# Kernel optimization log

Hardware: AMD Instinct MI355X
Metric: run time of the kernel (lower is better)

The kernel has to match this reference:

```python
import jax, jax.numpy as jnp
import numpy as np

H = 256
LATENT = 128
NODE_FEATS = (12, 5, 4)
EDGE_FEATS = (5, 4)
END_NODE = NODE_FEATS[0] - 1
MAX_NODES = 64


def setup_inputs() -> dict:
    key = jax.random.key(0)
    ks = iter(jax.random.split(key, 40))
    def rn(shape, s=0.1):
        return jax.random.normal(next(ks), shape, dtype=jnp.float32) * s
    inp = {
        "z": jax.random.normal(next(ks), (1, LATENT), dtype=jnp.float32),
        "lp_w": rn((H, LATENT)), "lp_b": rn((H,)),
        "nWih": rn((3 * H, H)), "nWhh": rn((3 * H, H)), "nbih": rn((3 * H,)), "nbhh": rn((3 * H,)),
        "eWih": rn((3 * H, H)), "eWhh": rn((3 * H, H)), "ebih": rn((3 * H,)), "ebhh": rn((3 * H,)),
    }
    for j, f in enumerate(NODE_FEATS):
        inp[f"nc{j}_w"] = rn((f, H)); inp[f"nc{j}_b"] = rn((f,))
    for j, f in enumerate(EDGE_FEATS):
        inp[f"ec{j}_w"] = rn((f, H)); inp[f"ec{j}_b"] = rn((f,))
    inp["max_nodes"] = MAX_NODES
    return inp


def _gru(x, h, Wih, Whh, bih, bhh):
    # torch.nn.GRU single step, single layer. x,h: (1,H)
    gi = x @ Wih.T + bih
    gh = h @ Whh.T + bhh
    ir, iz, inn = jnp.split(gi, 3, axis=-1)
    hr, hz, hn = jnp.split(gh, 3, axis=-1)
    r = jax.nn.sigmoid(ir + hr)
    zg = jax.nn.sigmoid(iz + hz)
    n = jnp.tanh(inn + r * hn)
    return (1.0 - zg) * n + zg * h


def _classify(emb, W, b):
    # Linear -> softmax -> (max prob, argmax), batch=1 -> scalars
    p = jax.nn.softmax(emb @ W.T + b, axis=-1)[0]
    return jnp.max(p), jnp.argmax(p)


def _generate(z, lp_w, lp_b, nWih, nWhh, nbih, nbhh, eWih, eWhh, ebih, ebhh,
              nc0_w, nc0_b, nc1_w, nc1_b, nc2_w, nc2_b,
              ec0_w, ec0_b, ec1_w, ec1_b, max_nodes):
    node_cls = ((nc0_w, nc0_b), (nc1_w, nc1_b), (nc2_w, nc2_b))
    edge_cls = ((ec0_w, ec0_b), (ec1_w, ec1_b))
    h0 = z @ lp_w.T + lp_b                     # latent_project; set_context
    buf0 = jnp.zeros((max_nodes, 1, H), z.dtype)  # node embedding history

    def step(carry, i):
        h, buf, done = carry
        x = jnp.where(i == 0, jnp.zeros((1, H), z.dtype), buf[jnp.maximum(i - 1, 0)])
        h1 = _gru(x, h, nWih, nWhh, nbih, nbhh)   # node_celli.forward_unit; emb = h1
        nps, nis = zip(*[_classify(h1, W, b) for W, b in node_cls])
        nprobs = jnp.stack(nps)                   # (3,)
        nidxs = jnp.stack(nis)                    # (3,) int
        is_end = nidxs[0] == END_NODE

        # edge cell: seq over previous node embeddings, most recent first
        def estep(he, t):
            valid = t < i
            src = jnp.clip(i - 1 - t, 0, max_nodes - 1)
            he2 = _gru(buf[src], he, eWih, eWhh, ebih, ebhh)
            he_new = jnp.where(valid, he2, he)
            eps, eis = zip(*[_classify(he_new, W, b) for W, b in edge_cls])
            return he_new, (jnp.stack(eps), jnp.stack(eis))

        he_fin, (ep_t, ei_t) = jax.lax.scan(estep, h1, jnp.arange(max_nodes))
        # reindex: edge for source node j was produced at inner step t = i-1-j
        js = jnp.arange(max_nodes)
        ts = jnp.clip(i - 1 - js, 0, max_nodes - 1)
        ep_row = ep_t[ts]                          # (max_nodes, 2)
        ei_row = ei_t[ts]
        vj = js < i
        no_edges = jnp.all(jnp.where(vj, ei_row[:, 0] == 0, True)) & (i > 0)

        active = jnp.logical_not(done)
        node_ok = active & jnp.logical_not(is_end) & jnp.logical_not(no_edges)
        done_new = done | is_end | no_edges

        h_next = jnp.where(node_ok & (i > 0), he_fin, h1)  # node hidden <- edge hidden
        h_next = jnp.where(active, h_next, h)
        buf_new = buf.at[i].set(jnp.where(node_ok, h1, buf[i]))

        edge_valid = vj & node_ok & (i > 0)
        out = (jnp.where(node_ok, nprobs, 0.0), nidxs, node_ok,
               jnp.where(edge_valid[:, None], ep_row, 0.0), ei_row, edge_valid)
        return (h_next, buf_new, done_new), out

    _, outs = jax.lax.scan(step, (h0, buf0, jnp.zeros((), bool)), jnp.arange(max_nodes))
    # node_probs (M,3), node_idxs (M,3), node_valid (M,),
    # edge_probs (M,M,2), edge_idxs (M,M,2), edge_valid (M,M)
    return outs


def reference(z, lp_w, lp_b, nWih, nWhh, nbih, nbhh, eWih, eWhh, ebih, ebhh,
              nc0_w, nc0_b, nc1_w, nc1_b, nc2_w, nc2_b,
              ec0_w, ec0_b, ec1_w, ec1_b, max_nodes):
    return _generate(z, lp_w, lp_b, nWih, nWhh, nbih, nbhh, eWih, eWhh, ebih, ebhh,
                     nc0_w, nc0_b, nc1_w, nc1_b, nc2_w, nc2_b,
                     ec0_w, ec0_b, ec1_w, ec1_b, max_nodes)
```

## Files before the change

### kernel.cpp

```cpp
#include <hip/hip_runtime.h>
#include <stdint.h>
#include <cstddef>


typedef unsigned int u32;

#define H 256
#define HL 128
#define G3 768
#define NW 16
#define SL 16
#define MAXN 64
#define NSTATE (1 + MAXN + (MAXN*(MAXN-1))/2)
#define SENTU 0xFFFFFFFFu
#define DEADV 0x0000DEADu
#define PAD 264

#define WG_CLS NW
#define WG_HELP0 (NW+1)
#define NHELP_PER 6
#define NROLE (WG_HELP0 + 2*NHELP_PER)
#define NWG 256

#define NP_OFF 0
#define NI_OFF 192
#define NV_OFF 384
#define EP_OFF 448
#define EI_OFF (EP_OFF + MAXN*MAXN*2)
#define EV_OFF (EI_OFF + MAXN*MAXN*2)

struct Wksp {
  float hP[NSTATE][H];
  float hS[NSTATE][H];
  float gi_e[MAXN][G3];
  float gi_n[MAXN][G3];
  u32 decP[MAXN];
  u32 decS[MAXN];
  u32 winner;
  u32 padw[7];
  u32 ticket[8];
};

union Shm {
  struct {
    float whe[3*SL*PAD];
    float whn[3*SL*PAD];
    float hcur[2][H];
    float bihe[3*SL], bhhe[3*SL], bihn[3*SL], bhhn[3*SL];
    float zv[HL];
    u32 dec;
  } w;
  struct {
    float cw[30*H];
    float cb[30];
    float hc[2][H];
    float logits[32];
    float np[3]; int ni[3];
    float ept[MAXN][2];
    int   eit[MAXN][2];
    u32 isend, bflag;
  } c;
  struct { float h1[H]; } hp;
};

__device__ __forceinline__ u32 ld_sc0(const u32* p) {
  u32 v;
  asm volatile("global_load_dword %0, %1, off sc0\n\ts_waitcnt vmcnt(0)"
               : "=&v"(v) : "v"(p) : "memory");
  return v;
}
__device__ __forceinline__ void st_sc0(u32* p, u32 v) {
  asm volatile("global_store_dword %0, %1, off sc0" :: "v"(p), "v"(v) : "memory");
}
__device__ __forceinline__ u32 ld_ag(const u32* p) {
  return __hip_atomic_load(p, __ATOMIC_RELAXED, __HIP_MEMORY_SCOPE_AGENT);
}
__device__ __forceinline__ void st_ag(u32* p, u32 v) {
  __hip_atomic_store(p, v, __ATOMIC_RELAXED, __HIP_MEMORY_SCOPE_AGENT);
}
__device__ __forceinline__ void pub2(u32* pp, u32* sp, u32 v, bool sc) {
  if (sc) st_sc0(pp, v);
  st_ag(sp, v);
}
__device__ __forceinline__ u32 spin2(const u32* pp, const u32* sp, bool sc) {
  if (sc) {
    #pragma unroll 1
    for (int i = 0; i < 16; ++i) {
      const u32 v = ld_sc0(pp);
      if (v != SENTU) return v;
    }
  }
  u32 v = ld_ag(sp);
  while (v == SENTU) v = ld_ag(sp);
  return v;
}
__device__ __forceinline__ float spin2f(const float* pp, const float* sp, bool sc) {
  return __uint_as_float(spin2((const u32*)pp, (const u32*)sp, sc));
}
__device__ __forceinline__ float spinf(const float* p) {
  u32 v = ld_ag((const u32*)p);
  while (v == SENTU) v = ld_ag((const u32*)p);
  return __uint_as_float(v);
}
__device__ __forceinline__ float spinf_slow(const float* p) {
  u32 v = ld_ag((const u32*)p);
  while (v == SENTU) {
    __builtin_amdgcn_s_sleep(1);
    v = ld_ag((const u32*)p);
  }
  return __uint_as_float(v);
}
__device__ __forceinline__ void pubf(float* p, float x) { st_ag((u32*)p, __float_as_uint(x)); }
__device__ __forceinline__ float sigm(float x) { return 1.0f / (1.0f + expf(-x)); }

__global__ __launch_bounds__(256)
void Generator_34746285425383_kernel(
    const float* __restrict__ z, const float* __restrict__ lp_w, const float* __restrict__ lp_b,
    const float* __restrict__ nWih, const float* __restrict__ nWhh,
    const float* __restrict__ nbih, const float* __restrict__ nbhh,
    const float* __restrict__ eWih, const float* __restrict__ eWhh,
    const float* __restrict__ ebih, const float* __restrict__ ebhh,
    const float* __restrict__ nc0w, const float* __restrict__ nc0b,
    const float* __restrict__ nc1w, const float* __restrict__ nc1b,
    const float* __restrict__ nc2w, const float* __restrict__ nc2b,
    const float* __restrict__ ec0w, const float* __restrict__ ec0b,
    const float* __restrict__ ec1w, const float* __restrict__ ec1b,
    float* __restrict__ out, Wksp* __restrict__ ws)
{
  __shared__ Shm S;
  __shared__ int role_s, mode_s;
  const int tid = threadIdx.x;

  if (tid == 0) {
    u32 xcc;
    asm volatile("s_getreg_b32 %0, hwreg(HW_REG_XCC_ID)" : "=s"(xcc));
    xcc &= 7u;
    const u32 slot = __hip_atomic_fetch_add(&ws->ticket[xcc], 1u,
                        __ATOMIC_RELAXED, __HIP_MEMORY_SCOPE_AGENT);
    if (slot == NROLE - 1) {
      u32 exp = SENTU;
      __hip_atomic_compare_exchange_strong(&ws->winner, &exp, xcc,
          __ATOMIC_RELAXED, __ATOMIC_RELAXED, __HIP_MEMORY_SCOPE_AGENT);
    }
    u32 wv = ld_ag(&ws->winner);
    int iters = 0;
    while (wv == SENTU) {
      ++iters;
      if (iters > 1500 && blockIdx.x == 0) {
        u32 exp = SENTU;
        __hip_atomic_compare_exchange_strong(&ws->winner, &exp, DEADV,
            __ATOMIC_RELAXED, __ATOMIC_RELAXED, __HIP_MEMORY_SCOPE_AGENT);
      }
      wv = ld_ag(&ws->winner);
    }
    if (wv <= 7u) { role_s = (wv == xcc && slot < NROLE) ? (int)slot : -1; mode_s = 1; }
    else          { role_s = ((int)blockIdx.x < NROLE) ? (int)blockIdx.x : -1; mode_s = 0; }
  }
  __syncthreads();
  const int bid = role_s;
  const bool sc = (mode_s != 0);
  if (bid < 0) return;

  if (bid < NW) {
    const int w = bid, g = tid >> 4, c = tid & 15;
    const int k = w * SL + g;
    const bool gl = (c < 2);
    for (int r = 0; r < 3 * SL; ++r) {
      const int gate = r / SL, gg = r % SL;
      const int grow = gate * H + (w * SL + gg);
      for (int col = tid; col < H; col += 256) {
        S.w.whe[r * PAD + col] = eWhh[grow * H + col];
        S.w.whn[r * PAD + col] = nWhh[grow * H + col];
      }
    }
    if (tid < 3 * SL) {
      const int gate = tid / SL, gg = tid % SL;
      const int grow = gate * H + w * SL + gg;
      S.w.bihe[tid] = ebih[grow]; S.w.bhhe[tid] = ebhh[grow];
      S.w.bihn[tid] = nbih[grow]; S.w.bhhn[tid] = nbhh[grow];
    }
    if (tid < HL) S.w.zv[tid] = z[tid];
    __syncthreads();

    {
      float p = 0.f;
      for (int it = 0; it < 8; ++it) {
        const int col = c + 16 * it;
        p += S.w.zv[col] * lp_w[k * HL + col];
      }
      for (int off = 1; off < 16; off <<= 1) p += __shfl_xor(p, off);
      const float h0 = p + lp_b[k];
      if (c == 0 && sc) st_sc0((u32*)&ws->hP[0][k], __float_as_uint(h0));
      if (c == 1)       st_ag((u32*)&ws->hS[0][k], __float_as_uint(h0));
    }

    int m = 1, idx_carry = 0;
    bool done = false;
    unsigned long long valid = 0ull;
    float pg0 = 0.f, pg1 = 0.f, pg2 = 0.f;
    const float* pga = nullptr;

    for (int i = 0; i < MAXN; ++i) {
      for (int t = -1; t < i; ++t) {
        const bool is_node = (t < 0);
        const int hidx = is_node ? idx_carry : (m - 1);
        const int src  = is_node ? (i - 1) : (i - 1 - t);
        float* hc = S.w.hcur[m & 1];
        hc[tid] = spin2f(&ws->hP[hidx][tid], &ws->hS[hidx][tid], sc);
        float gi0 = 0.f, gi1 = 0.f, gi2 = 0.f;
        const bool use_gi = (src >= 0) && ((valid >> src) & 1ull);
        if (gl && use_gi) {
          gi0 = pg0; gi1 = pg1; gi2 = pg2;
          if (__float_as_uint(gi0) == SENTU) gi0 = spinf(&pga[0 * H + k]);
          if (__float_as_uint(gi1) == SENTU) gi1 = spinf(&pga[1 * H + k]);
          if (__float_as_uint(gi2) == SENTU) gi2 = spinf(&pga[2 * H + k]);
        }
        __syncthreads();
        const float* Wl = is_node ? S.w.whn : S.w.whe;
        float p0 = 0.f, p1 = 0.f, p2 = 0.f;
        #pragma unroll
        for (int it = 0; it < 16; ++it) {
          const int col = c + 16 * it;
          const float hv = hc[col];
          p0 += Wl[(0 * SL + g) * PAD + col] * hv;
          p1 += Wl[(1 * SL + g) * PAD + col] * hv;
          p2 += Wl[(2 * SL + g) * PAD + col] * hv;
        }
        for (int off = 1; off < 16; off <<= 1) {
          p0 += __shfl_xor(p0, off);
          p1 += __shfl_xor(p1, off);
          p2 += __shfl_xor(p2, off);
        }
        const float* bih = is_node ? S.w.bihn : S.w.bihe;
        const float* bhh = is_node ? S.w.bhhn : S.w.bhhe;
        const float rr = sigm(gi0 + bih[0 * SL + g] + p0 + bhh[0 * SL + g]);
        const float zz = sigm(gi1 + bih[1 * SL + g] + p1 + bhh[1 * SL + g]);
        const float nn = tanhf(gi2 + bih[2 * SL + g] + rr * (p2 + bhh[2 * SL + g]));
        const float hp = (1.f - zz) * nn + zz * hc[k];
        if (c == 0 && sc) st_sc0((u32*)&ws->hP[m][k], __float_as_uint(hp));
        if (c == 1)       st_ag((u32*)&ws->hS[m][k], __float_as_uint(hp));
        if (gl) {
          int ni = i, nt = t + 1;
          if (nt >= i) { ni = i + 1; nt = -1; }
          if (ni < MAXN) {
            const bool nnode = (nt < 0);
            const int nsrc = nnode ? (ni - 1) : (ni - 1 - nt);
            if (nsrc >= 0) {
              pga = nnode ? ws->gi_n[nsrc] : ws->gi_e[nsrc];
              pg0 = __builtin_nontemporal_load(&pga[0 * H + k]);
              pg1 = __builtin_nontemporal_load(&pga[1 * H + k]);
              pg2 = __builtin_nontemporal_load(&pga[2 * H + k]);
            }
          }
        }
        ++m;
      }
      if (tid == 0) S.w.dec = spin2(&ws->decP[i], &ws->decS[i], sc);
      __syncthreads();
      const u32 dec = S.w.dec;
      const bool is_end   = (dec >> 1) & 1u;
      const bool no_edges = (dec >> 2) & 1u;
      const bool active   = !done;
      const bool node_ok  = active && !is_end && !no_edges;
      if (node_ok) valid |= (1ull << i);
      const int s_end = m - 1, node_m = m - 1 - i;
      if (active) idx_carry = (node_ok && i > 0) ? s_end : node_m;
      done = done || is_end || no_edges;
    }

  } else if (bid == WG_CLS) {
    const int g = tid >> 4, c = tid & 15;
    const float* wsrc[5] = { nc0w, nc1w, nc2w, ec0w, ec1w };
    const float* bsrc[5] = { nc0b, nc1b, nc2b, ec0b, ec1b };
    const int hbase[5] = { 0, 12, 17, 21, 26 };
    const int hlen[5]  = { 12, 5, 4, 5, 4 };
    for (int hh = 0; hh < 5; ++hh)
      for (int r = 0; r < hlen[hh]; ++r)
        for (int col = tid; col < H; col += 256)
          S.c.cw[(hbase[hh] + r) * H + col] = wsrc[hh][r * H + col];
    if (tid < 30) {
      const int hh = tid < 12 ? 0 : tid < 17 ? 1 : tid < 21 ? 2 : tid < 26 ? 3 : 4;
      S.c.cb[tid] = bsrc[hh][tid - hbase[hh]];
    }
    __syncthreads();

    int m = 1;
    bool done = false;
    for (int i = 0; i < MAXN; ++i) {
      for (int t = -1; t < i; ++t) {
        float* hcb = S.c.hc[m & 1];
        hcb[tid] = spin2f(&ws->hP[m][tid], &ws->hS[m][tid], sc);
        __syncthreads();
        for (int rsel = 0; rsel < 2; ++rsel) {
          const int r = g + 16 * rsel;
          float p = 0.f;
          if (r < 30) {
            #pragma unroll
            for (int it = 0; it < 16; ++it) {
              const int col = c + 16 * it;
              p += S.c.cw[r * H + col] * hcb[col];
            }
          }
          for (int off = 1; off < 16; off <<= 1) p += __shfl_xor(p, off);
          if (r < 30 && c == 0) S.c.logits[r] = p + S.c.cb[r];
        }
        __syncthreads();
        if (tid < 64) {
          const int lane = tid;
          int hh, j;
          if (lane < 16)      { hh = 0; j = lane;      }
          else if (lane < 24) { hh = 1; j = lane - 16; }
          else if (lane < 32) { hh = 2; j = lane - 24; }
          else if (lane < 40) { hh = 3; j = lane - 32; }
          else if (lane < 48) { hh = 4; j = lane - 40; }
          else                { hh = 4; j = 99; }
          const int hb = hbase[hh], hl = hlen[hh];
          const bool live = (j < hl);
          const float myl = live ? S.c.logits[hb + j] : -3.4e38f;
          float mx = myl; int idx = live ? j : 1000;
          #pragma unroll
          for (int mk = 1; mk <= 4; mk <<= 1) {
            const float lv = __shfl_xor(mx, mk);
            const int   iv = __shfl_xor(idx, mk);
            if (lv > mx || (lv == mx && iv < idx)) { mx = lv; idx = iv; }
          }
          { const float lv = __shfl_xor(mx, 8);
            const int   iv = __shfl_xor(idx, 8);
            if (lane < 16 && (lv > mx || (lv == mx && iv < idx))) { mx = lv; idx = iv; } }
          float e = live ? expf(myl - mx) : 0.f;
          #pragma unroll
          for (int mk = 1; mk <= 4; mk <<= 1) e += __shfl_xor(e, mk);
          { const float ev = __shfl_xor(e, 8); if (lane < 16) e += ev; }
          const float pm = 1.0f / e;
          if (t < 0) {
            if (lane == 0)  { S.c.np[0] = pm; S.c.ni[0] = idx;
                              S.c.isend = (idx == 11) ? 1u : 0u; }
            if (lane == 16) { S.c.np[1] = pm; S.c.ni[1] = idx; }
            if (lane == 24) { S.c.np[2] = pm; S.c.ni[2] = idx; }
            if (i == 0) {
              if (lane == 32) { S.c.ept[0][0] = pm; S.c.eit[0][0] = idx; }
              if (lane == 40) { S.c.ept[0][1] = pm; S.c.eit[0][1] = idx; }
            }
          } else {
            if (lane == 32) { S.c.ept[t][0] = pm; S.c.eit[t][0] = idx; }
            if (lane == 40) { S.c.ept[t][1] = pm; S.c.eit[t][1] = idx; }
          }
        }
        ++m;
      }
      __syncthreads();
      if (tid < 64) {
        const bool myok = (tid < i) ? (S.c.eit[tid][0] == 0) : true;
        const unsigned long long b = __ballot(myok);
        if (tid == 0) S.c.bflag = ((b == ~0ull) && (i > 0)) ? 1u : 0u;
      }
      __syncthreads();
      const bool is_end   = (S.c.isend != 0u);
      const bool no_edges = (S.c.bflag != 0u);
      const bool active   = !done;
      const bool node_ok  = active && !is_end && !no_edges;
      if (tid == 0) {
        const u32 d = 1u | (is_end ? 2u : 0u) | (no_edges ? 4u : 0u);
        pub2(&ws->decP[i], &ws->decS[i], d, sc);
      }
      if (tid < MAXN) {
        const int j = tid;
        const bool vj = j < i;
        const bool ev = vj && node_ok && (i > 0);
        const int tt = vj ? (i - 1 - j) : 0;
        out[EP_OFF + (i * MAXN + j) * 2 + 0] = ev ? S.c.ept[tt][0] : 0.f;
        out[EP_OFF + (i * MAXN + j) * 2 + 1] = ev ? S.c.ept[tt][1] : 0.f;
        out[EI_OFF + (i * MAXN + j) * 2 + 0] = (float)S.c.eit[tt][0];
        out[EI_OFF + (i * MAXN + j) * 2 + 1] = (float)S.c.eit[tt][1];
        out[EV_OFF + i * MAXN + j] = ev ? 1.f : 0.f;
      } else if (tid < MAXN + 8) {
        const int q = tid - MAXN;
        if (q < 3)       out[NP_OFF + i * 3 + q]       = node_ok ? S.c.np[q] : 0.f;
        else if (q < 6)  out[NI_OFF + i * 3 + (q - 3)] = (float)S.c.ni[q - 3];
        else if (q == 6) out[NV_OFF + i]               = node_ok ? 1.f : 0.f;
      }
      done = done || is_end || no_edges;
      __syncthreads();
    }

  } else {
    const int e = bid - WG_HELP0;
    const bool is_edge = (e < NHELP_PER);
    const int rowbase = (e % NHELP_PER) * 128;
    const float* Wih = is_edge ? eWih : nWih;
    float* gdst = is_edge ? &ws->gi_e[0][0] : &ws->gi_n[0][0];
    const int g = tid >> 4, c = tid & 15;
    int m_node = 1;
    for (int i = 0; i < MAXN; ++i) {
      S.hp.h1[tid] = spinf_slow(&ws->hS[m_node][tid]);
      __syncthreads();
      for (int rr = 0; rr < 8; ++rr) {
        const int row = rowbase + g * 8 + rr;
        float p = 0.f;
        #pragma unroll
        for (int u = 0; u < 4; ++u) {
          const float4 wv = *(const float4*)&Wih[row * H + c * 16 + u * 4];
          p += wv.x * S.hp.h1[c * 16 + u * 4 + 0]
             + wv.y * S.hp.h1[c * 16 + u * 4 + 1]
             + wv.z * S.hp.h1[c * 16 + u * 4 + 2]
             + wv.w * S.hp.h1[c * 16 + u * 4 + 3];
        }
        for (int off = 1; off < 16; off <<= 1) p += __shfl_xor(p, off);
        if (c == 0) pubf(&gdst[i * G3 + row], p);
      }
      __syncthreads();
      m_node += 1 + i;
    }
  }
}

extern "C" void kernel_launch(void* const* d_in, const int* in_sizes, int n_in,
                              void* d_out, int out_size, void* d_ws, size_t ws_size,
                              hipStream_t stream) {
  hipMemsetAsync(d_ws, 0xFF, offsetof(Wksp, ticket), stream);
  hipMemsetAsync((char*)d_ws + offsetof(Wksp, ticket), 0,
                 sizeof(Wksp) - offsetof(Wksp, ticket), stream);
  Generator_34746285425383_kernel<<<dim3(NWG), dim3(256), 0, stream>>>(
      (const float*)d_in[0],  (const float*)d_in[1],  (const float*)d_in[2],
      (const float*)d_in[3],  (const float*)d_in[4],  (const float*)d_in[5],
      (const float*)d_in[6],  (const float*)d_in[7],  (const float*)d_in[8],
      (const float*)d_in[9],  (const float*)d_in[10],
      (const float*)d_in[11], (const float*)d_in[12],
      (const float*)d_in[13], (const float*)d_in[14],
      (const float*)d_in[15], (const float*)d_in[16],
      (const float*)d_in[17], (const float*)d_in[18],
      (const float*)d_in[19], (const float*)d_in[20],
      (float*)d_out, (Wksp*)d_ws);
}
```

Baseline: 5.048 ms.

## Keep GRU and classifier weights in registers instead of LDS

Recurrent Whh rows for the node and edge GRUs, and the classifier weight rows, are now loaded once into per-thread register arrays instead of shared memory, so each step's matvec reads only the hidden vector from LDS. A large dummy shared array pins one workgroup per CU, and launch bounds are set to one block per CU so the compiler can use the extra registers. The aim is to shorten the latency-bound per-step dot products on the serial critical path. The risk is register pressure (96 weight registers per thread) causing spills.

```diff
diff --git a/kernel.cpp b/kernel.cpp
--- a/kernel.cpp
+++ b/kernel.cpp
@@ -14,7 +14,6 @@
 #define NSTATE (1 + MAXN + (MAXN*(MAXN-1))/2)
 #define SENTU 0xFFFFFFFFu
 #define DEADV 0x0000DEADu
-#define PAD 264
 
 #define WG_CLS NW
 #define WG_HELP0 (NW+1)
@@ -42,16 +41,14 @@
 };
 
 union Shm {
+  float force[26624];
   struct {
-    float whe[3*SL*PAD];
-    float whn[3*SL*PAD];
     float hcur[2][H];
     float bihe[3*SL], bhhe[3*SL], bihn[3*SL], bhhn[3*SL];
     float zv[HL];
     u32 dec;
   } w;
   struct {
-    float cw[30*H];
     float cb[30];
     float hc[2][H];
     float logits[32];
@@ -113,7 +110,7 @@
 __device__ __forceinline__ void pubf(float* p, float x) { st_ag((u32*)p, __float_as_uint(x)); }
 __device__ __forceinline__ float sigm(float x) { return 1.0f / (1.0f + expf(-x)); }
 
-__global__ __launch_bounds__(256)
+__global__ __launch_bounds__(256, 1)
 void Generator_34746285425383_kernel(
     const float* __restrict__ z, const float* __restrict__ lp_w, const float* __restrict__ lp_b,
     const float* __restrict__ nWih, const float* __restrict__ nWhh,
@@ -165,13 +162,16 @@
     const int w = bid, g = tid >> 4, c = tid & 15;
     const int k = w * SL + g;
     const bool gl = (c < 2);
-    for (int r = 0; r < 3 * SL; ++r) {
-      const int gate = r / SL, gg = r % SL;
-      const int grow = gate * H + (w * SL + gg);
-      for (int col = tid; col < H; col += 256) {
-        S.w.whe[r * PAD + col] = eWhh[grow * H + col];
-        S.w.whn[r * PAD + col] = nWhh[grow * H + col];
-      }
+    float wn0[16], wn1[16], wn2[16], we0[16], we1[16], we2[16];
+    #pragma unroll
+    for (int it = 0; it < 16; ++it) {
+      const int col = c + 16 * it;
+      wn0[it] = nWhh[(0 * H + k) * H + col];
+      wn1[it] = nWhh[(1 * H + k) * H + col];
+      wn2[it] = nWhh[(2 * H + k) * H + col];
+      we0[it] = eWhh[(0 * H + k) * H + col];
+      we1[it] = eWhh[(1 * H + k) * H + col];
+      we2[it] = eWhh[(2 * H + k) * H + col];
     }
     if (tid < 3 * SL) {
       const int gate = tid / SL, gg = tid % SL;
@@ -216,15 +216,19 @@
           if (__float_as_uint(gi2) == SENTU) gi2 = spinf(&pga[2 * H + k]);
         }
         __syncthreads();
-        const float* Wl = is_node ? S.w.whn : S.w.whe;
         float p0 = 0.f, p1 = 0.f, p2 = 0.f;
-        #pragma unroll
-        for (int it = 0; it < 16; ++it) {
-          const int col = c + 16 * it;
-          const float hv = hc[col];
-          p0 += Wl[(0 * SL + g) * PAD + col] * hv;
-          p1 += Wl[(1 * SL + g) * PAD + col] * hv;
-          p2 += Wl[(2 * SL + g) * PAD + col] * hv;
+        if (is_node) {
+          #pragma unroll
+          for (int it = 0; it < 16; ++it) {
+            const float hv = hc[c + 16 * it];
+            p0 += wn0[it] * hv; p1 += wn1[it] * hv; p2 += wn2[it] * hv;
+          }
+        } else {
+          #pragma unroll
+          for (int it = 0; it < 16; ++it) {
+            const float hv = hc[c + 16 * it];
+            p0 += we0[it] * hv; p1 += we1[it] * hv; p2 += we2[it] * hv;
+          }
         }
         for (int off = 1; off < 16; off <<= 1) {
           p0 += __shfl_xor(p0, off);
@@ -273,11 +277,24 @@
     const float* wsrc[5] = { nc0w, nc1w, nc2w, ec0w, ec1w };
     const float* bsrc[5] = { nc0b, nc1b, nc2b, ec0b, ec1b };
     const int hbase[5] = { 0, 12, 17, 21, 26 };
-    const int hlen[5]  = { 12, 5, 4, 5, 4 };
-    for (int hh = 0; hh < 5; ++hh)
-      for (int r = 0; r < hlen[hh]; ++r)
-        for (int col = tid; col < H; col += 256)
-          S.c.cw[(hbase[hh] + r) * H + col] = wsrc[hh][r * H + col];
+    float cw0[16], cw1[16];
+    {
+      const int r0 = g;
+      const int h0i = r0 < 12 ? 0 : r0 < 17 ? 1 : r0 < 21 ? 2 : r0 < 26 ? 3 : 4;
+      const float* W0 = wsrc[h0i];
+      const int rr0 = r0 - hbase[h0i];
+      const int r1 = g + 16;
+      const int h1i = r1 < 17 ? 1 : r1 < 21 ? 2 : r1 < 26 ? 3 : 4;
+      const float* W1 = wsrc[h1i];
+      const int rr1 = r1 - hbase[h1i];
+      const bool live1 = (r1 < 30);
+      #pragma unroll
+      for (int it = 0; it < 16; ++it) {
+        const int col = c + 16 * it;
+        cw0[it] = W0[rr0 * H + col];
+        cw1[it] = live1 ? W1[rr1 * H + col] : 0.f;
+      }
+    }
     if (tid < 30) {
       const int hh = tid < 12 ? 0 : tid < 17 ? 1 : tid < 21 ? 2 : tid < 26 ? 3 : 4;
       S.c.cb[tid] = bsrc[hh][tid - hbase[hh]];
@@ -291,18 +308,22 @@
         float* hcb = S.c.hc[m & 1];
         hcb[tid] = spin2f(&ws->hP[m][tid], &ws->hS[m][tid], sc);
         __syncthreads();
-        for (int rsel = 0; rsel < 2; ++rsel) {
-          const int r = g + 16 * rsel;
-          float p = 0.f;
-          if (r < 30) {
-            #pragma unroll
-            for (int it = 0; it < 16; ++it) {
-              const int col = c + 16 * it;
-              p += S.c.cw[r * H + col] * hcb[col];
-            }
-          }
-          for (int off = 1; off < 16; off <<= 1) p += __shfl_xor(p, off);
-          if (r < 30 && c == 0) S.c.logits[r] = p + S.c.cb[r];
+        {
+          float p0 = 0.f, p1 = 0.f;
+          #pragma unroll
+          for (int it = 0; it < 16; ++it) {
+            const float hv = hcb[c + 16 * it];
+            p0 += cw0[it] * hv;
+            p1 += cw1[it] * hv;
+          }
+          for (int off = 1; off < 16; off <<= 1) {
+            p0 += __shfl_xor(p0, off);
+            p1 += __shfl_xor(p1, off);
+          }
+          if (c == 0) {
+            S.c.logits[g] = p0 + S.c.cb[g];
+            if (g + 16 < 30) S.c.logits[g + 16] = p1 + S.c.cb[g + 16];
+          }
         }
         __syncthreads();
         if (tid < 64) {
@@ -314,7 +335,8 @@
           else if (lane < 40) { hh = 3; j = lane - 32; }
           else if (lane < 48) { hh = 4; j = lane - 40; }
           else                { hh = 4; j = 99; }
-          const int hb = hbase[hh], hl = hlen[hh];
+          const int hb = hbase[hh];
+          const int hl = hh == 0 ? 12 : hh == 1 ? 5 : hh == 2 ? 4 : hh == 3 ? 5 : 4;
           const bool live = (j < hl);
           const float myl = live ? S.c.logits[hb + j] : -3.4e38f;
           float mx = myl; int idx = live ? j : 1000;
```

Result: faster. 4.594 ms, median of 2 (-9.0%).
